# Kernel optimization log

Hardware: AMD Instinct MI355X
Metric: run time of the kernel (lower is better)

## Reference

```python
import jax, jax.numpy as jnp
import numpy as np

D_MODEL = 1024
N_HEADS = 16
D_FF = 4096
B, T = 4, 2048
EPS = 1e-5


def layernorm(x, g, b):
    mu = jnp.mean(x, axis=-1, keepdims=True)
    var = jnp.var(x, axis=-1, keepdims=True)
    return (x - mu) * jax.lax.rsqrt(var + EPS) * g + b


def setup_inputs() -> dict:
    key = jax.random.key(0)
    ks = jax.random.split(key, 8)
    s = 0.02
    return {
        "x": jax.random.normal(ks[0], (B, T, D_MODEL), jnp.float32),
        "ln1_g": jnp.ones((D_MODEL,), jnp.float32),
        "ln1_b": jnp.zeros((D_MODEL,), jnp.float32),
        "wq": jax.random.normal(ks[1], (D_MODEL, D_MODEL), jnp.float32) * s,
        "bq": jnp.zeros((D_MODEL,), jnp.float32),
        "wk": jax.random.normal(ks[2], (D_MODEL, D_MODEL), jnp.float32) * s,
        "bk": jnp.zeros((D_MODEL,), jnp.float32),
        "wv": jax.random.normal(ks[3], (D_MODEL, D_MODEL), jnp.float32) * s,
        "bv": jnp.zeros((D_MODEL,), jnp.float32),
        "wo": jax.random.normal(ks[4], (D_MODEL, D_MODEL), jnp.float32) * s,
        "bo": jnp.zeros((D_MODEL,), jnp.float32),
        "ln2_g": jnp.ones((D_MODEL,), jnp.float32),
        "ln2_b": jnp.zeros((D_MODEL,), jnp.float32),
        "w1": jax.random.normal(ks[5], (D_FF, D_MODEL), jnp.float32) * s,
        "b1": jnp.zeros((D_FF,), jnp.float32),
        "w2": jax.random.normal(ks[6], (D_MODEL, D_FF), jnp.float32) * s,
        "b2": jnp.zeros((D_MODEL,), jnp.float32),
    }


def reference(x, ln1_g, ln1_b, wq, bq, wk, bk, wv, bv, wo, bo,
              ln2_g, ln2_b, w1, b1, w2, b2):
    d_k = D_MODEL // N_HEADS
    # --- attention sublayer (pre-LN) ---
    h = layernorm(x, ln1_g, ln1_b)                       # [B,T,D]
    q = (h @ wq.T + bq).reshape(B, T, N_HEADS, d_k)
    k = (h @ wk.T + bk).reshape(B, T, N_HEADS, d_k)
    v = (h @ wv.T + bv).reshape(B, T, N_HEADS, d_k)
    scores = jnp.einsum("bqhd,bkhd->bhqk", q, k) / jnp.sqrt(jnp.float32(d_k))
    attn = jax.nn.softmax(scores, axis=-1)               # [B,H,T,T]
    o = jnp.einsum("bhqk,bkhd->bqhd", attn, v).reshape(B, T, D_MODEL)
    x = x + (o @ wo.T + bo)
    # --- FFN sublayer ---
    h2 = layernorm(x, ln2_g, ln2_b)
    h2 = jax.nn.gelu(h2 @ w1.T + b1, approximate=False)  # torch GELU = exact erf
    x = x + (h2 @ w2.T + b2)
    return x
```

## Files before the change

kernel.cpp:

```cpp
#include <hip/hip_runtime.h>
#include <math.h>


#define D_MODEL 1024
#define D_FF    4096
#define NH      16
#define BATCH   4
#define SEQ     2048
#define DK      64
#define MTOK    (BATCH*SEQ)
#define NBH     (BATCH*NH)

typedef __bf16 bf16;
typedef _Float16 f16;
typedef bf16  bf16x4 __attribute__((ext_vector_type(4)));
typedef bf16  bf16x8 __attribute__((ext_vector_type(8)));
typedef f16   f16x4  __attribute__((ext_vector_type(4)));
typedef f16   f16x8  __attribute__((ext_vector_type(8)));
typedef __fp16 hf16x2 __attribute__((ext_vector_type(2)));
typedef __fp16 hf16x4 __attribute__((ext_vector_type(4)));
typedef __fp16 hf16x8 __attribute__((ext_vector_type(8)));
typedef float f32x4  __attribute__((ext_vector_type(4)));

__device__ __forceinline__ void gload_lds16(const void* g, void* l) {
  __builtin_amdgcn_global_load_lds(
      (__attribute__((address_space(1))) void*)g,
      (__attribute__((address_space(3))) void*)l, 16, 0, 0);
}

#define BAR() __builtin_amdgcn_s_barrier()
#define WAIT_VM0() do { asm volatile("s_waitcnt vmcnt(0)" ::: "memory"); \
  __builtin_amdgcn_sched_barrier(0); } while (0)
#define WAIT_LGKM0() do { asm volatile("s_waitcnt lgkmcnt(0)" ::: "memory"); } while (0)

__global__ __launch_bounds__(256) void cast_w(const float* __restrict__ s,
                                              bf16* __restrict__ d, int n) {
  int i = (blockIdx.x * 256 + threadIdx.x) * 4;
  if (i >= n) return;
  float4 v = *(const float4*)(s + i);
  bf16x4 o;
  o[0] = (bf16)v.x; o[1] = (bf16)v.y; o[2] = (bf16)v.z; o[3] = (bf16)v.w;
  *(bf16x4*)(d + i) = o;
}

__global__ __launch_bounds__(256) void ln_kernel(const float* __restrict__ x,
                                                 const float* __restrict__ g,
                                                 const float* __restrict__ b,
                                                 bf16* __restrict__ out) {
  int row = blockIdx.x;
  int tid = threadIdx.x;
  const float* xr = x + (size_t)row * D_MODEL;
  float4 v = *(const float4*)(xr + tid * 4);
  float s  = v.x + v.y + v.z + v.w;
  float sq = v.x*v.x + v.y*v.y + v.z*v.z + v.w*v.w;
  #pragma unroll
  for (int off = 1; off < 64; off <<= 1) {
    s  += __shfl_xor(s,  off, 64);
    sq += __shfl_xor(sq, off, 64);
  }
  __shared__ float ls[4], lq[4];
  int wid = tid >> 6, lane = tid & 63;
  if (lane == 0) { ls[wid] = s; lq[wid] = sq; }
  __syncthreads();
  s  = ls[0] + ls[1] + ls[2] + ls[3];
  sq = lq[0] + lq[1] + lq[2] + lq[3];
  float mu   = s * (1.0f / D_MODEL);
  float var  = sq * (1.0f / D_MODEL) - mu * mu;
  float rstd = rsqrtf(var + 1e-5f);
  float4 gv = *(const float4*)(g + tid * 4);
  float4 bv = *(const float4*)(b + tid * 4);
  bf16x4 o;
  o[0] = (bf16)((v.x - mu) * rstd * gv.x + bv.x);
  o[1] = (bf16)((v.y - mu) * rstd * gv.y + bv.y);
  o[2] = (bf16)((v.z - mu) * rstd * gv.z + bv.z);
  o[3] = (bf16)((v.w - mu) * rstd * gv.w + bv.w);
  *(bf16x4*)(out + (size_t)row * D_MODEL + tid * 4) = o;
}

enum { EP_QKV = 0, EP_RESID = 1, EP_GELU = 2 };

#define QSCALE 0.18033688011112042f

template <int EP, int CFG>
__global__ __launch_bounds__(512) void gemm8p(
    const bf16* __restrict__ A, const bf16* __restrict__ W,
    const float* __restrict__ bias,
    const float* __restrict__ resid,
    float* __restrict__ out_f32,
    bf16* __restrict__ out_bf,
    int M, int N, int K) {
  constexpr int BM  = CFG ? 128 : 256;
  constexpr int BK  = CFG ? 64 : 32;
  constexpr int WM  = CFG ? 64 : 128;
  constexpr int FRN = WM / 16;
  constexpr int FRP = FRN / 2;
  constexpr int KKN = BK / 32;
  constexpr int RB  = BK * 2;
  constexpr int GR  = RB / 16;
  constexpr int RSH = CFG ? 7 : 6;
  constexpr int AB  = 16384;
  constexpr int TB  = AB + 256 * BK * 2;
  constexpr int L   = TB / 8192;
  constexpr int Lh  = L / 2;

  __shared__ char lds[3 * TB];

  int tiles_n = N >> 8;
  int nwg = (M / BM) * tiles_n;
  int bid = blockIdx.x;
  int swz = (bid & 7) * (nwg >> 3) + (bid >> 3);
  int bm = swz / tiles_n, bn = swz % tiles_n;
  int m0 = bm * BM, n0 = bn << 8;
  int tid = threadIdx.x, wid = tid >> 6, lane = tid & 63;
  int wm = wid >> 2, wn = wid & 3;
  int l15 = lane & 15, l4 = lane >> 4;

  f32x4 acc[FRN][4];
  #pragma unroll
  for (int i = 0; i < FRN; i++)
    #pragma unroll
    for (int j = 0; j < 4; j++)
      #pragma unroll
      for (int e = 0; e < 4; e++) acc[i][j][e] = 0.f;

  auto STAGE = [&](int kt, int nb, int part) {
    char* buf = lds + nb * TB;
    #pragma unroll
    for (int l = part * Lh; l < part * Lh + Lh; ++l) {
      bool isA = l < 2;
      int o = (isA ? l : l - 2) * 8192 + tid * 16;
      int row = o >> RSH;
      int g = (o >> 4) & (GR - 1);
      int gs = g ^ (CFG ? (row & 7) : ((row >> 1) & 3));
      const bf16* src = (isA ? A + (size_t)(m0 + row) * K
                             : W + (size_t)(n0 + row) * K) + kt * BK + gs * 8;
      gload_lds16(src, buf + (isA ? 0 : AB) + o);
    }
  };

  int nt = K / BK;
  STAGE(0, 0, 0); STAGE(0, 0, 1);
  STAGE(1, 1, 0); STAGE(1, 1, 1);
  if constexpr (CFG) { asm volatile("s_waitcnt vmcnt(6)" ::: "memory"); }
  else               { asm volatile("s_waitcnt vmcnt(4)" ::: "memory"); }
  __builtin_amdgcn_sched_barrier(0);
  BAR();

  bf16x8 bfr[4][KKN];
  for (int t = 0; t < nt; ++t) {
    int cb = t % 3, nb = cb >= 1 ? cb - 1 : 2;
    bool ds_ = (t + 2) < nt;
    const char* bc = lds + cb * TB;

    bf16x8 af[FRP][KKN];
    #pragma unroll
    for (int f = 0; f < FRP; ++f)
      #pragma unroll
      for (int kk = 0; kk < KKN; ++kk) {
        int row = wm * WM + f * 16 + l15;
        int g = (kk * 4 + l4) ^ (CFG ? (row & 7) : ((row >> 1) & 3));
        af[f][kk] = *(const bf16x8*)(bc + row * RB + g * 16);
      }
    #pragma unroll
    for (int fc = 0; fc < 4; ++fc)
      #pragma unroll
      for (int kk = 0; kk < KKN; ++kk) {
        int row = wn * 64 + fc * 16 + l15;
        int g = (kk * 4 + l4) ^ (CFG ? (row & 7) : ((row >> 1) & 3));
        bfr[fc][kk] = *(const bf16x8*)(bc + AB + row * RB + g * 16);
      }
    if (ds_) STAGE(t + 2, nb, 0);
    BAR();
    WAIT_LGKM0();
    __builtin_amdgcn_s_setprio(1);
    #pragma unroll
    for (int f = 0; f < FRP; ++f)
      #pragma unroll
      for (int fc = 0; fc < 4; ++fc)
        #pragma unroll
        for (int kk = 0; kk < KKN; ++kk)
          acc[f][fc] = __builtin_amdgcn_mfma_f32_16x16x32_bf16(af[f][kk], bfr[fc][kk],
                                                               acc[f][fc], 0, 0, 0);
    __builtin_amdgcn_s_setprio(0);
    BAR();

    bf16x8 af1[FRP][KKN];
    #pragma unroll
    for (int f = 0; f < FRP; ++f)
      #pragma unroll
      for (int kk = 0; kk < KKN; ++kk) {
        int row = wm * WM + (FRP + f) * 16 + l15;
        int g = (kk * 4 + l4) ^ (CFG ? (row & 7) : ((row >> 1) & 3));
        af1[f][kk] = *(const bf16x8*)(bc + row * RB + g * 16);
      }
    if (ds_) STAGE(t + 2, nb, 1);
    BAR();
    WAIT_LGKM0();
    __builtin_amdgcn_s_setprio(1);
    #pragma unroll
    for (int f = 0; f < FRP; ++f)
      #pragma unroll
      for (int fc = 0; fc < 4; ++fc)
        #pragma unroll
        for (int kk = 0; kk < KKN; ++kk)
          acc[FRP + f][fc] = __builtin_amdgcn_mfma_f32_16x16x32_bf16(af1[f][kk], bfr[fc][kk],
                                                                     acc[FRP + f][fc], 0, 0, 0);
    __builtin_amdgcn_s_setprio(0);
    if (t < nt - 2) {
      if constexpr (CFG) { asm volatile("s_waitcnt vmcnt(6)" ::: "memory"); }
      else               { asm volatile("s_waitcnt vmcnt(4)" ::: "memory"); }
      __builtin_amdgcn_sched_barrier(0);
    } else if (t == nt - 2) {
      WAIT_VM0();
    }
    BAR();
  }

  if (EP == EP_QKV) {
    #pragma unroll
    for (int i = 0; i < FRN; i++)
      #pragma unroll
      for (int j = 0; j < 4; j++) {
        int gm0 = m0 + wm * WM + i * 16 + (l4 << 2);
        int gn  = n0 + wn * 64 + j * 16 + l15;
        int which = gn >> 10;
        int nn = gn & 1023, head = nn >> 6, d = nn & 63;
        int bb = gm0 >> 11, t = gm0 & 2047;
        float bv = bias[gn];
        if (which == 2) {
          int sbase = (t & ~31) + ((t >> 2) & 3) * 8 + ((t >> 4) & 1) * 4;
          f16x4 pk;
          #pragma unroll
          for (int jj = 0; jj < 4; jj++) pk[jj] = (f16)(acc[i][j][jj] + bv);
          *(f16x4*)((f16*)out_bf + (size_t)2 * NBH * SEQ * DK +
                    ((size_t)(bb * NH + head) * DK + d) * SEQ + sbase) = pk;
        } else {
          float scale = (which == 0) ? QSCALE : 1.0f;
          #pragma unroll
          for (int jj = 0; jj < 4; jj++) {
            float cv = (acc[i][j][jj] + bv) * scale;
            size_t idx = (size_t)which * (NBH * SEQ * DK) +
                         ((size_t)(bb * NH + head) * SEQ + (t + jj)) * DK + d;
            out_bf[idx] = (bf16)cv;
          }
        }
      }
  } else {
    #pragma unroll
    for (int i = 0; i < FRN; i++)
      #pragma unroll
      for (int j = 0; j < 4; j++)
        #pragma unroll
        for (int jj = 0; jj < 4; jj++) {
          int gm = m0 + wm * WM + i * 16 + (l4 << 2) + jj;
          int gn = n0 + wn * 64 + j * 16 + l15;
          float cv = acc[i][j][jj] + bias[gn];
          if (EP == EP_RESID) {
            size_t idx = (size_t)gm * N + gn;
            out_f32[idx] = resid[idx] + cv;
          } else {
            float ge = 0.5f * cv * (1.0f + erff(cv * 0.70710678118654752f));
            out_bf[(size_t)gm * N + gn] = (bf16)ge;
          }
        }
  }
}

__global__ __launch_bounds__(512) void attn_kernel(
    const bf16* __restrict__ q, const bf16* __restrict__ k,
    const f16* __restrict__ vt, bf16* __restrict__ o) {
  __shared__ bf16 kt_lds[2][128 * 64];
  __shared__ f16  vt_lds[2][64 * 128];
  int bid = blockIdx.x;
  int swzb = (bid & 7) * 128 + (bid >> 3);
  int bh = swzb >> 4;
  int qt = swzb & 15;
  int t0 = qt << 7;
  int tid = threadIdx.x, wid = tid >> 6, lane = tid & 63;
  int l15 = lane & 15, l4 = lane >> 4;

  int kb0 = l15 * 128 + ((l4 ^ (l15 & 7)) << 4);
  int kb1 = l15 * 128 + (((4 + l4) ^ (l15 & 7)) << 4);
  int vb32[4];
  #pragma unroll
  for (int n = 0; n < 4; n++)
    vb32[n] = l15 * 256 + (((n * 4 + l4) ^ (l15 & 7)) << 4);

  const bf16* qbase = q + ((size_t)bh * SEQ + t0 + wid * 16 + l15) * DK;
  bf16x8 qf[2];
  qf[0] = *(const bf16x8*)(qbase + (l4 << 3));
  qf[1] = *(const bf16x8*)(qbase + 32 + (l4 << 3));

  f16x8 vones8;
  #pragma unroll
  for (int e = 0; e < 8; e++) vones8[e] = (f16)1.f;
  float m_run = -1e30f;
  f32x4 acc_o[4];
  f32x4 acc_l;
  #pragma unroll
  for (int nd = 0; nd < 4; nd++)
    #pragma unroll
    for (int e = 0; e < 4; e++) acc_o[nd][e] = 0.f;
  #pragma unroll
  for (int e = 0; e < 4; e++) acc_l[e] = 0.f;

  const bf16* gKsrc[2];
  const f16*  gVsrc[2];
  #pragma unroll
  for (int it = 0; it < 2; ++it) {
    int o = it * 8192 + tid * 16;
    int rowk = o >> 7, gk = (o >> 4) & 7;
    gKsrc[it] = k + ((size_t)bh * SEQ + rowk) * DK + ((gk ^ (rowk & 7)) << 3);
    int d = o >> 8, gd = (o >> 4) & 15;
    gVsrc[it] = vt + ((size_t)bh * DK + d) * SEQ + ((gd ^ (d & 7)) << 3);
  }

  auto stage = [&](int buf, int t) {
    int kv0 = t * 128;
    char* dK = (char*)&kt_lds[buf][0] + tid * 16;
    char* dV = (char*)&vt_lds[buf][0] + tid * 16;
    #pragma unroll
    for (int it = 0; it < 2; ++it) {
      gload_lds16(gKsrc[it] + (size_t)kv0 * DK, dK + it * 8192);
      gload_lds16(gVsrc[it] + kv0, dV + it * 8192);
    }
  };

  stage(0, 0);
  WAIT_VM0();
  BAR();

  for (int t = 0; t < SEQ / 128; ++t) {
    int cur = t & 1;
    if (t < SEQ / 128 - 1) stage(cur ^ 1, t + 1);
    const char* kbase = (const char*)&kt_lds[cur][0];
    const char* vbase = (const char*)&vt_lds[cur][0];

    f32x4 accs[8];
    #pragma unroll
    for (int n = 0; n < 8; n++)
      #pragma unroll
      for (int e = 0; e < 4; e++) accs[n][e] = 0.f;
    __builtin_amdgcn_s_setprio(1);
    #pragma unroll
    for (int n = 0; n < 8; n++) {
      bf16x8 kf0 = *(const bf16x8*)(kbase + kb0 + n * 2048);
      bf16x8 kf1 = *(const bf16x8*)(kbase + kb1 + n * 2048);
      accs[n] = __builtin_amdgcn_mfma_f32_16x16x32_bf16(kf0, qf[0], accs[n], 0, 0, 0);
      accs[n] = __builtin_amdgcn_mfma_f32_16x16x32_bf16(kf1, qf[1], accs[n], 0, 0, 0);
    }
    __builtin_amdgcn_s_setprio(0);

    float mloc = -1e30f;
    #pragma unroll
    for (int n = 0; n < 8; n++) {
      float a0 = fmaxf(accs[n][0], accs[n][1]);
      float a1 = fmaxf(accs[n][2], accs[n][3]);
      mloc = fmaxf(mloc, fmaxf(a0, a1));
    }
    float mt = fmaxf(mloc, __shfl_xor(mloc, 16, 64));
    mt = fmaxf(mt, __shfl_xor(mt, 32, 64));
    if (__any(mt > m_run + 8.0f)) {
      float mn = fmaxf(m_run, mt);
      float sc = __builtin_amdgcn_exp2f(m_run - mn);
      m_run = mn;
      float scr0 = __shfl(sc, l4 * 20 + 0, 64);
      float scr1 = __shfl(sc, l4 * 20 + 1, 64);
      float scr2 = __shfl(sc, l4 * 20 + 2, 64);
      float scr3 = __shfl(sc, l4 * 20 + 3, 64);
      #pragma unroll
      for (int nd = 0; nd < 4; nd++) {
        acc_o[nd][0] *= scr0; acc_o[nd][1] *= scr1;
        acc_o[nd][2] *= scr2; acc_o[nd][3] *= scr3;
      }
      acc_l[0] *= scr0; acc_l[1] *= scr1; acc_l[2] *= scr2; acc_l[3] *= scr3;
    }
    f16x8 pa32[4];
    #pragma unroll
    for (int n = 0; n < 4; n++) {
      float e0 = __builtin_amdgcn_exp2f(accs[2*n][0] - m_run);
      float e1 = __builtin_amdgcn_exp2f(accs[2*n][1] - m_run);
      float e2 = __builtin_amdgcn_exp2f(accs[2*n][2] - m_run);
      float e3 = __builtin_amdgcn_exp2f(accs[2*n][3] - m_run);
      float e4 = __builtin_amdgcn_exp2f(accs[2*n+1][0] - m_run);
      float e5 = __builtin_amdgcn_exp2f(accs[2*n+1][1] - m_run);
      float e6 = __builtin_amdgcn_exp2f(accs[2*n+1][2] - m_run);
      float e7 = __builtin_amdgcn_exp2f(accs[2*n+1][3] - m_run);
      hf16x2 p01 = __builtin_amdgcn_cvt_pkrtz(e0, e1);
      hf16x2 p23 = __builtin_amdgcn_cvt_pkrtz(e2, e3);
      hf16x2 p45 = __builtin_amdgcn_cvt_pkrtz(e4, e5);
      hf16x2 p67 = __builtin_amdgcn_cvt_pkrtz(e6, e7);
      hf16x4 lo = __builtin_shufflevector(p01, p23, 0, 1, 2, 3);
      hf16x4 hi = __builtin_shufflevector(p45, p67, 0, 1, 2, 3);
      hf16x8 cmb = __builtin_shufflevector(lo, hi, 0, 1, 2, 3, 4, 5, 6, 7);
      pa32[n] = __builtin_bit_cast(f16x8, cmb);
    }

    __builtin_amdgcn_s_setprio(1);
    #pragma unroll
    for (int n = 0; n < 4; n++) {
      #pragma unroll
      for (int nd = 0; nd < 4; nd++) {
        f16x8 vf = *(const f16x8*)(vbase + vb32[n] + nd * 4096);
        acc_o[nd] = __builtin_amdgcn_mfma_f32_16x16x32_f16(pa32[n], vf, acc_o[nd], 0, 0, 0);
      }
      acc_l = __builtin_amdgcn_mfma_f32_16x16x32_f16(pa32[n], vones8, acc_l, 0, 0, 0);
    }
    __builtin_amdgcn_s_setprio(0);

    if (t < SEQ / 128 - 1) { WAIT_VM0(); }
    BAR();
  }

  float rl0 = 1.0f / acc_l[0], rl1 = 1.0f / acc_l[1];
  float rl2 = 1.0f / acc_l[2], rl3 = 1.0f / acc_l[3];
  int bb = bh >> 4, hh = bh & 15;
  #pragma unroll
  for (int nd = 0; nd < 4; nd++) {
    int d = nd * 16 + l15;
    int rowb = t0 + wid * 16 + l4 * 4;
    o[((size_t)bb * SEQ + rowb + 0) * D_MODEL + hh * DK + d] = (bf16)(acc_o[nd][0] * rl0);
    o[((size_t)bb * SEQ + rowb + 1) * D_MODEL + hh * DK + d] = (bf16)(acc_o[nd][1] * rl1);
    o[((size_t)bb * SEQ + rowb + 2) * D_MODEL + hh * DK + d] = (bf16)(acc_o[nd][2] * rl2);
    o[((size_t)bb * SEQ + rowb + 3) * D_MODEL + hh * DK + d] = (bf16)(acc_o[nd][3] * rl3);
  }
}

extern "C" void kernel_launch(void* const* d_in, const int* in_sizes, int n_in,
                              void* d_out, int out_size, void* d_ws, size_t ws_size,
                              hipStream_t stream) {
  const float* x    = (const float*)d_in[0];
  const float* ln1g = (const float*)d_in[1];
  const float* ln1b = (const float*)d_in[2];
  const float* wq   = (const float*)d_in[3];
  const float* bq   = (const float*)d_in[4];
  const float* wk   = (const float*)d_in[5];
  const float* bk   = (const float*)d_in[6];
  const float* wv   = (const float*)d_in[7];
  const float* bv   = (const float*)d_in[8];
  const float* wo   = (const float*)d_in[9];
  const float* bo   = (const float*)d_in[10];
  const float* ln2g = (const float*)d_in[11];
  const float* ln2b = (const float*)d_in[12];
  const float* w1   = (const float*)d_in[13];
  const float* b1   = (const float*)d_in[14];
  const float* w2   = (const float*)d_in[15];
  const float* b2   = (const float*)d_in[16];
  float* out = (float*)d_out;

  char* ws = (char*)d_ws;
  bf16* wqkv_b = (bf16*)(ws);
  bf16* wo_b   = (bf16*)(ws + ((size_t)6  << 20));
  bf16* w1_b   = (bf16*)(ws + ((size_t)8  << 20));
  bf16* w2_b   = (bf16*)(ws + ((size_t)16 << 20));
  bf16* h_b    = (bf16*)(ws + ((size_t)24 << 20));
  bf16* qkv_b  = (bf16*)(ws + ((size_t)40 << 20));
  bf16* o_b    = (bf16*)(ws + ((size_t)88 << 20));
  bf16* ffn1_b = (bf16*)(ws + ((size_t)40 << 20));
  float* bqkv  = (float*)(ws + ((size_t)104 << 20));

  cast_w<<<1024, 256, 0, stream>>>(wq, wqkv_b, 1 << 20);
  cast_w<<<1024, 256, 0, stream>>>(wk, wqkv_b + (1 << 20), 1 << 20);
  cast_w<<<1024, 256, 0, stream>>>(wv, wqkv_b + (2 << 20), 1 << 20);
  cast_w<<<1024, 256, 0, stream>>>(wo, wo_b, 1 << 20);
  cast_w<<<4096, 256, 0, stream>>>(w1, w1_b, 1 << 22);
  cast_w<<<4096, 256, 0, stream>>>(w2, w2_b, 1 << 22);
  (void)hipMemcpyAsync(bqkv,        bq, 4096, hipMemcpyDeviceToDevice, stream);
  (void)hipMemcpyAsync(bqkv + 1024, bk, 4096, hipMemcpyDeviceToDevice, stream);
  (void)hipMemcpyAsync(bqkv + 2048, bv, 4096, hipMemcpyDeviceToDevice, stream);

  ln_kernel<<<MTOK, 256, 0, stream>>>(x, ln1g, ln1b, h_b);
  gemm8p<EP_QKV, 1><<<768, 512, 0, stream>>>(h_b, wqkv_b, bqkv, nullptr, nullptr,
                                             qkv_b, MTOK, 3072, 1024);
  attn_kernel<<<NBH * 16, 512, 0, stream>>>(qkv_b, qkv_b + (size_t)NBH * SEQ * DK,
                                            (const f16*)(qkv_b + (size_t)2 * NBH * SEQ * DK),
                                            o_b);
  gemm8p<EP_RESID, 1><<<256, 512, 0, stream>>>(o_b, wo_b, bo, x, out, nullptr,
                                               MTOK, 1024, 1024);
  ln_kernel<<<MTOK, 256, 0, stream>>>(out, ln2g, ln2b, h_b);
  gemm8p<EP_GELU, 0><<<512, 512, 0, stream>>>(h_b, w1_b, b1, nullptr, nullptr,
                                              ffn1_b, MTOK, 4096, 1024);
  gemm8p<EP_RESID, 1><<<256, 512, 0, stream>>>(ffn1_b, w2_b, b2, out, out, nullptr,
                                               MTOK, 1024, 4096);
}
```

Measured before the change: 420.0 us.

## Collapse two-phase ping-pong GEMM main loop into single-phase loop

Replaces the split main loop, which loaded half of the A fragments, issued half of the prefetch, synced and ran half of the MFMAs, then repeated for the second half, with a single phase per k-tile. The whole next-next tile is prefetched at the top, all A and B fragments are read from LDS, and all MFMAs run, with one barrier per iteration. This removes three barriers and the explicit lgkmcnt waits per iteration. It gives up the finer interleaving of LDS reads, global prefetch and MFMA work across waves, and raises register pressure because all A fragments are live at once.

```diff
diff --git a/kernel.cpp b/kernel.cpp
--- a/kernel.cpp
+++ b/kernel.cpp
@@ -31,7 +31,6 @@
 #define BAR() __builtin_amdgcn_s_barrier()
 #define WAIT_VM0() do { asm volatile("s_waitcnt vmcnt(0)" ::: "memory"); \
   __builtin_amdgcn_sched_barrier(0); } while (0)
-#define WAIT_LGKM0() do { asm volatile("s_waitcnt lgkmcnt(0)" ::: "memory"); } while (0)
 
 __global__ __launch_bounds__(256) void cast_w(const float* __restrict__ s,
                                               bf16* __restrict__ d, int n) {
@@ -93,7 +92,6 @@
   constexpr int BK  = CFG ? 64 : 32;
   constexpr int WM  = CFG ? 64 : 128;
   constexpr int FRN = WM / 16;
-  constexpr int FRP = FRN / 2;
   constexpr int KKN = BK / 32;
   constexpr int RB  = BK * 2;
   constexpr int GR  = RB / 16;
@@ -101,7 +99,6 @@
   constexpr int AB  = 16384;
   constexpr int TB  = AB + 256 * BK * 2;
   constexpr int L   = TB / 8192;
-  constexpr int Lh  = L / 2;
 
   __shared__ char lds[3 * TB];
 
@@ -123,10 +120,10 @@
       #pragma unroll
       for (int e = 0; e < 4; e++) acc[i][j][e] = 0.f;
 
-  auto STAGE = [&](int kt, int nb, int part) {
+  auto STAGE = [&](int kt, int nb) {
     char* buf = lds + nb * TB;
     #pragma unroll
-    for (int l = part * Lh; l < part * Lh + Lh; ++l) {
+    for (int l = 0; l < L; ++l) {
       bool isA = l < 2;
       int o = (isA ? l : l - 2) * 8192 + tid * 16;
       int row = o >> RSH;
@@ -139,22 +136,22 @@
   };
 
   int nt = K / BK;
-  STAGE(0, 0, 0); STAGE(0, 0, 1);
-  STAGE(1, 1, 0); STAGE(1, 1, 1);
+  STAGE(0, 0);
+  STAGE(1, 1);
   if constexpr (CFG) { asm volatile("s_waitcnt vmcnt(6)" ::: "memory"); }
   else               { asm volatile("s_waitcnt vmcnt(4)" ::: "memory"); }
   __builtin_amdgcn_sched_barrier(0);
   BAR();
 
-  bf16x8 bfr[4][KKN];
   for (int t = 0; t < nt; ++t) {
     int cb = t % 3, nb = cb >= 1 ? cb - 1 : 2;
-    bool ds_ = (t + 2) < nt;
     const char* bc = lds + cb * TB;
 
-    bf16x8 af[FRP][KKN];
-    #pragma unroll
-    for (int f = 0; f < FRP; ++f)
+    if (t + 2 < nt) STAGE(t + 2, nb);
+
+    bf16x8 af[FRN][KKN], bfr[4][KKN];
+    #pragma unroll
+    for (int f = 0; f < FRN; ++f)
       #pragma unroll
       for (int kk = 0; kk < KKN; ++kk) {
         int row = wm * WM + f * 16 + l15;
@@ -169,12 +166,10 @@
         int g = (kk * 4 + l4) ^ (CFG ? (row & 7) : ((row >> 1) & 3));
         bfr[fc][kk] = *(const bf16x8*)(bc + AB + row * RB + g * 16);
       }
-    if (ds_) STAGE(t + 2, nb, 0);
-    BAR();
-    WAIT_LGKM0();
+
     __builtin_amdgcn_s_setprio(1);
     #pragma unroll
-    for (int f = 0; f < FRP; ++f)
+    for (int f = 0; f < FRN; ++f)
       #pragma unroll
       for (int fc = 0; fc < 4; ++fc)
         #pragma unroll
@@ -182,35 +177,12 @@
           acc[f][fc] = __builtin_amdgcn_mfma_f32_16x16x32_bf16(af[f][kk], bfr[fc][kk],
                                                                acc[f][fc], 0, 0, 0);
     __builtin_amdgcn_s_setprio(0);
-    BAR();
-
-    bf16x8 af1[FRP][KKN];
-    #pragma unroll
-    for (int f = 0; f < FRP; ++f)
-      #pragma unroll
-      for (int kk = 0; kk < KKN; ++kk) {
-        int row = wm * WM + (FRP + f) * 16 + l15;
-        int g = (kk * 4 + l4) ^ (CFG ? (row & 7) : ((row >> 1) & 3));
-        af1[f][kk] = *(const bf16x8*)(bc + row * RB + g * 16);
-      }
-    if (ds_) STAGE(t + 2, nb, 1);
-    BAR();
-    WAIT_LGKM0();
-    __builtin_amdgcn_s_setprio(1);
-    #pragma unroll
-    for (int f = 0; f < FRP; ++f)
-      #pragma unroll
-      for (int fc = 0; fc < 4; ++fc)
-        #pragma unroll
-        for (int kk = 0; kk < KKN; ++kk)
-          acc[FRP + f][fc] = __builtin_amdgcn_mfma_f32_16x16x32_bf16(af1[f][kk], bfr[fc][kk],
-                                                                     acc[FRP + f][fc], 0, 0, 0);
-    __builtin_amdgcn_s_setprio(0);
-    if (t < nt - 2) {
+
+    if (t + 2 < nt) {
       if constexpr (CFG) { asm volatile("s_waitcnt vmcnt(6)" ::: "memory"); }
       else               { asm volatile("s_waitcnt vmcnt(4)" ::: "memory"); }
       __builtin_amdgcn_sched_barrier(0);
-    } else if (t == nt - 2) {
+    } else if (t + 1 < nt) {
       WAIT_VM0();
     }
     BAR();
```

Result: no change. 418.9 us (-0.3%).
